# Optimization experiments

Measured on AMD Instinct MI355X. Metric: run time of the kernel, lower is better.

Reference implementation:

```python
import jax, jax.numpy as jnp
import numpy as np

B, S, HID = 1, 2048, 2048
NH, NKV, HD = 32, 8, 64
SCALE = HD ** -0.5


def _rotary_tables(seq_len, dim, base=10000.0):
    inv_freq = 1.0 / (base ** (jnp.arange(0, dim, 2, dtype=jnp.float32) / dim))
    t = jnp.arange(seq_len, dtype=jnp.float32)
    freqs = jnp.outer(t, inv_freq)                      # [S, D/2]
    emb = jnp.concatenate([freqs, freqs], axis=-1)      # [S, D]
    return jnp.cos(emb)[None], jnp.sin(emb)[None]       # [1, S, D]


def setup_inputs() -> dict:
    key = jax.random.key(0)
    ks = jax.random.split(key, 5)
    cos, sin = _rotary_tables(S, HD)
    std = HID ** -0.5
    return {
        "hidden_states": jax.random.normal(ks[0], (B, S, HID), jnp.float32),
        "cos": cos,
        "sin": sin,
        "Wq": jax.random.normal(ks[1], (HID, NH * HD), jnp.float32) * std,
        "Wk": jax.random.normal(ks[2], (HID, NKV * HD), jnp.float32) * std,
        "Wv": jax.random.normal(ks[3], (HID, NKV * HD), jnp.float32) * std,
        "Wo": jax.random.normal(ks[4], (NH * HD, HID), jnp.float32) * std,
    }


def _rotate_half(x):
    x1, x2 = jnp.split(x, 2, axis=-1)
    return jnp.concatenate([-x2, x1], axis=-1)


def reference(hidden_states, cos, sin, Wq, Wk, Wv, Wo):
    b, s, _ = hidden_states.shape
    # projections -> [B, H, S, D]
    q = (hidden_states @ Wq).reshape(b, s, NH, HD).transpose(0, 2, 1, 3)
    k = (hidden_states @ Wk).reshape(b, s, NKV, HD).transpose(0, 2, 1, 3)
    v = (hidden_states @ Wv).reshape(b, s, NKV, HD).transpose(0, 2, 1, 3)
    # rotary embedding (broadcast over heads)
    c = cos[:, None, :, :]
    sn = sin[:, None, :, :]
    q = q * c + _rotate_half(q) * sn
    k = k * c + _rotate_half(k) * sn
    # GQA: repeat kv heads
    groups = NH // NKV
    k = jnp.repeat(k, groups, axis=1)
    v = jnp.repeat(v, groups, axis=1)
    scores = jnp.einsum("bhqd,bhkd->bhqk", q, k) * SCALE
    causal = jnp.tril(jnp.ones((s, s), dtype=bool))
    scores = jnp.where(causal, scores, jnp.finfo(scores.dtype).min)
    weights = jax.nn.softmax(scores, axis=-1)
    attn = jnp.einsum("bhqk,bhkd->bhqd", weights, v)
    attn = attn.transpose(0, 2, 1, 3).reshape(b, s, NH * HD)
    out = attn @ Wo
    return out, weights
```

## Files before the change

### kernel.cpp

```cpp
#include <hip/hip_runtime.h>

typedef short short8 __attribute__((ext_vector_type(8)));
typedef float f32x4 __attribute__((ext_vector_type(4)));

#define S_LEN 2048
#define HID 2048
#define NH 32
#define NKV 8
#define HD 64
#define DQKV 3072
#define SCALE 0.125f
#define SM_OFF 8.0f

static __device__ __forceinline__ unsigned short f2bf(float f) {
    unsigned int u = __float_as_uint(f);
    u += 0x7FFF + ((u >> 16) & 1);
    return (unsigned short)(u >> 16);
}
static __device__ __forceinline__ float bf2f(unsigned short u) {
    return __uint_as_float((unsigned int)u << 16);
}

#define GLDS16(g, l)                                                                     \
    __builtin_amdgcn_global_load_lds((const __attribute__((address_space(1))) unsigned int*)(g), \
                                     (__attribute__((address_space(3))) unsigned int*)(l), 16, 0, 0)

__global__ void prep(const float* __restrict__ Wq, const float* __restrict__ Wk,
                     const float* __restrict__ Wv, const float* __restrict__ Wo,
                     const float* __restrict__ hidden,
                     unsigned short* __restrict__ Wt, unsigned short* __restrict__ Wot,
                     unsigned short* __restrict__ Hb) {
    const int z = blockIdx.z;
    const int t = threadIdx.x;
    if (z == 4) {
        int idx = (blockIdx.y * 64 + blockIdx.x) * 256 + t;
        float4 v = ((const float4*)hidden)[idx];
        ushort4 o = {f2bf(v.x), f2bf(v.y), f2bf(v.z), f2bf(v.w)};
        ((ushort4*)Hb)[idx] = o;
        return;
    }
    const float* src; unsigned short* dst; int sld;
    if (z == 0)      { src = Wq; dst = Wt; sld = HID; }
    else if (z == 1) { if (blockIdx.x >= 16) return; src = Wk; dst = Wt + (size_t)2048 * HID; sld = 512; }
    else if (z == 2) { if (blockIdx.x >= 16) return; src = Wv; dst = Wt + (size_t)2560 * HID; sld = 512; }
    else             { src = Wo; dst = Wot; sld = HID; }
    __shared__ float tile[32][33];
    const int tx = t & 31, ty = t >> 5;
    const int r0 = blockIdx.y * 32, c0 = blockIdx.x * 32;
#pragma unroll
    for (int i = 0; i < 4; ++i)
        tile[ty * 4 + i][tx] = src[(size_t)(r0 + ty * 4 + i) * sld + c0 + tx];
    __syncthreads();
#pragma unroll
    for (int i = 0; i < 4; ++i)
        dst[(size_t)(c0 + ty * 4 + i) * HID + r0 + tx] = f2bf(tile[tx][ty * 4 + i]);
}

template <int MODE>
__global__ __launch_bounds__(512) void gemm_fused(const unsigned short* __restrict__ A,
                                                  const unsigned short* __restrict__ Bt,
                                                  float* __restrict__ C,
                                                  const float* __restrict__ cosb,
                                                  const float* __restrict__ sinb,
                                                  unsigned short* __restrict__ Qb,
                                                  unsigned short* __restrict__ Kb,
                                                  unsigned short* __restrict__ Vt,
                                                  int K, int lda, int ldb, int ldc) {
    __shared__ __align__(16) unsigned short As[128 * 64];
    __shared__ __align__(16) unsigned short Bs[128 * 64];
    const int t = threadIdx.x, lane = t & 63, wv = t >> 6;
    const int m0 = blockIdx.y * 128, n0 = blockIdx.x * 128;
    const int wm = wv >> 1, wn = wv & 1;
    const int lr = lane & 15, lg = lane >> 4;
    const int srow = lane >> 3;
    const int scol = ((lane & 7) ^ srow) * 8;
    f32x4 acc[2][4] = {};
    for (int k0 = 0; k0 < K; k0 += 64) {
        __syncthreads();
#pragma unroll
        for (int p = 0; p < 2; ++p) {
            int rbase = wv * 16 + p * 8;
            GLDS16(&A[(size_t)(m0 + rbase + srow) * lda + k0 + scol], &As[rbase * 64]);
            GLDS16(&Bt[(size_t)(n0 + rbase + srow) * ldb + k0 + scol], &Bs[rbase * 64]);
        }
        __syncthreads();
#pragma unroll
        for (int kk = 0; kk < 2; ++kk) {
            short8 a[2], b[4];
#pragma unroll
            for (int i = 0; i < 2; ++i) {
                int row = wm * 32 + i * 16 + lr;
                a[i] = *(const short8*)&As[row * 64 + (((kk * 4 + lg) ^ (row & 7)) * 8)];
            }
#pragma unroll
            for (int j = 0; j < 4; ++j) {
                int row = wn * 64 + j * 16 + lr;
                b[j] = *(const short8*)&Bs[row * 64 + (((kk * 4 + lg) ^ (row & 7)) * 8)];
            }
#pragma unroll
            for (int i = 0; i < 2; ++i)
#pragma unroll
                for (int j = 0; j < 4; ++j)
                    acc[i][j] = __builtin_amdgcn_mfma_f32_16x16x32_bf16(a[i], b[j], acc[i][j], 0, 0, 0);
        }
    }

    if (MODE == 1) {
#pragma unroll
        for (int i = 0; i < 2; ++i)
#pragma unroll
            for (int j = 0; j < 4; ++j)
#pragma unroll
                for (int r = 0; r < 4; ++r)
                    C[(size_t)(m0 + wm * 32 + i * 16 + lg * 4 + r) * ldc +
                      n0 + wn * 64 + j * 16 + lr] = acc[i][j][r];
        return;
    }

    const int head = (n0 + wn * 64) >> 6;
    if (head < NH + NKV) {
        unsigned short* dst = (head < NH) ? Qb : Kb;
        const int dld = (head < NH) ? HID : 512;
        const int hc = (head < NH) ? head * HD : (head - NH) * HD;
#pragma unroll
        for (int i = 0; i < 2; ++i) {
            const int s0 = m0 + wm * 32 + i * 16 + lg * 4;
#pragma unroll
            for (int j = 0; j < 2; ++j) {
                const int c = j * 16 + lr;
#pragma unroll
                for (int r = 0; r < 4; ++r) {
                    const int s = s0 + r;
                    float x1 = acc[i][j][r], x2 = acc[i][j + 2][r];
                    float c1 = cosb[s * HD + c],      s1 = sinb[s * HD + c];
                    float c2 = cosb[s * HD + c + 32], s2 = sinb[s * HD + c + 32];
                    dst[(size_t)s * dld + hc + c]      = f2bf(x1 * c1 - x2 * s1);
                    dst[(size_t)s * dld + hc + c + 32] = f2bf(x2 * c2 + x1 * s2);
                }
            }
        }
    } else {
        const int vh = head - NH - NKV;
#pragma unroll
        for (int i = 0; i < 2; ++i) {
            const int s0 = m0 + wm * 32 + i * 16 + lg * 4;
#pragma unroll
            for (int j = 0; j < 4; ++j) {
                const int d = vh * HD + j * 16 + lr;
                ushort4 o = {f2bf(acc[i][j][0]), f2bf(acc[i][j][1]),
                             f2bf(acc[i][j][2]), f2bf(acc[i][j][3])};
                *(ushort4*)&Vt[(size_t)d * S_LEN + s0] = o;
            }
        }
    }
}

__global__ __launch_bounds__(512, 2) void attn_fused(const unsigned short* __restrict__ Qb,
                                                     const unsigned short* __restrict__ Kb,
                                                     const unsigned short* __restrict__ Vt,
                                                     float* __restrict__ w,
                                                     unsigned short* __restrict__ Ab) {
    __shared__ __align__(16) unsigned short Ks[128 * 72];
    __shared__ __align__(16) unsigned short Vs[64 * 136];
    __shared__ __align__(16) unsigned short Ps[8][32 * 40];
    const int p = blockIdx.x, h = blockIdx.y, kvh = h >> 2;
    const int t = threadIdx.x, lane = t & 63, wv = t >> 6;
    const int grp = wv & 1, wr = wv >> 1;
    const int qt = grp ? (15 - p) : p;
    const int q0 = qt * 128;
    const int lr = lane & 15, lg = lane >> 4;
    const int ktmax = 15 - p;
    unsigned short* Pw = &Ps[wv][0];

    short8 qf[2][2];
#pragma unroll
    for (int i = 0; i < 2; ++i)
#pragma unroll
        for (int kk = 0; kk < 2; ++kk)
            qf[i][kk] = *(const short8*)&Qb[(size_t)(q0 + wr * 32 + i * 16 + lr) * HID +
                                            h * HD + kk * 32 + lg * 8];

    const int krow = t >> 2, kc = (t & 3) * 16;
    const int vrow = t >> 3, vc = (t & 7) * 16;

    float l_r[2] = {0.f, 0.f};

    for (int kt = 0; kt <= ktmax; ++kt) {
        __syncthreads();
        *(short8*)&Ks[krow * 72 + kc] =
            *(const short8*)&Kb[(size_t)(kt * 128 + krow) * 512 + kvh * HD + kc];
        *(short8*)&Ks[krow * 72 + kc + 8] =
            *(const short8*)&Kb[(size_t)(kt * 128 + krow) * 512 + kvh * HD + kc + 8];
        __syncthreads();
        if (kt > qt) continue;
        f32x4 acc[8][2] = {};
#pragma unroll
        for (int kk = 0; kk < 2; ++kk) {
            short8 af[8];
#pragma unroll
            for (int j = 0; j < 8; ++j)
                af[j] = *(const short8*)&Ks[(j * 16 + lr) * 72 + kk * 32 + lg * 8];
#pragma unroll
            for (int j = 0; j < 8; ++j)
#pragma unroll
                for (int i = 0; i < 2; ++i)
                    acc[j][i] = __builtin_amdgcn_mfma_f32_16x16x32_bf16(af[j], qf[i][kk], acc[j][i], 0, 0, 0);
        }
        const bool diag = (kt == qt);
#pragma unroll
        for (int i = 0; i < 2; ++i) {
            const int qg = q0 + wr * 32 + i * 16 + lr;
            float sum = 0.f;
#pragma unroll
            for (int j = 0; j < 8; ++j)
#pragma unroll
                for (int r = 0; r < 4; ++r) {
                    int kg = kt * 128 + j * 16 + lg * 4 + r;
                    float s = acc[j][i][r] * SCALE;
                    s = (!diag || kg <= qg) ? s : -1.0e30f;
                    sum += __expf(s - SM_OFF);
                }
            sum += __shfl_xor(sum, 16);
            sum += __shfl_xor(sum, 32);
            l_r[i] += sum;
        }
    }

    const float invl[2] = {1.f / l_r[0], 1.f / l_r[1]};

    f32x4 o[2][4] = {};
    for (int kt = 0; kt <= ktmax; ++kt) {
        __syncthreads();
        *(short8*)&Ks[krow * 72 + kc] =
            *(const short8*)&Kb[(size_t)(kt * 128 + krow) * 512 + kvh * HD + kc];
        *(short8*)&Ks[krow * 72 + kc + 8] =
            *(const short8*)&Kb[(size_t)(kt * 128 + krow) * 512 + kvh * HD + kc + 8];
        *(short8*)&Vs[vrow * 136 + vc] =
            *(const short8*)&Vt[(size_t)(kvh * HD + vrow) * S_LEN + kt * 128 + vc];
        *(short8*)&Vs[vrow * 136 + vc + 8] =
            *(const short8*)&Vt[(size_t)(kvh * HD + vrow) * S_LEN + kt * 128 + vc + 8];
        __syncthreads();
        if (kt <= qt) {
            f32x4 acc[8][2] = {};
#pragma unroll
            for (int kk = 0; kk < 2; ++kk) {
                short8 af[8];
#pragma unroll
                for (int j = 0; j < 8; ++j)
                    af[j] = *(const short8*)&Ks[(j * 16 + lr) * 72 + kk * 32 + lg * 8];
#pragma unroll
                for (int j = 0; j < 8; ++j)
#pragma unroll
                    for (int i = 0; i < 2; ++i)
                        acc[j][i] = __builtin_amdgcn_mfma_f32_16x16x32_bf16(af[j], qf[i][kk], acc[j][i], 0, 0, 0);
            }
            const bool diag = (kt == qt);
#pragma unroll
            for (int ks = 0; ks < 4; ++ks) {
#pragma unroll
                for (int i = 0; i < 2; ++i) {
                    const int qg = q0 + wr * 32 + i * 16 + lr;
#pragma unroll
                    for (int jj = 0; jj < 2; ++jj) {
                        const int j = ks * 2 + jj;
                        ushort4 pk;
#pragma unroll
                        for (int r = 0; r < 4; ++r) {
                            int kg = kt * 128 + j * 16 + lg * 4 + r;
                            float s = acc[j][i][r] * SCALE;
                            s = (!diag || kg <= qg) ? s : -1.0e30f;
                            ((unsigned short*)&pk)[r] = f2bf(__expf(s - SM_OFF) * invl[i]);
                        }
                        *(ushort4*)&Pw[(i * 16 + lr) * 40 + jj * 16 + lg * 4] = pk;
                    }
                }
                short8 pa[2], vb[4];
#pragma unroll
                for (int i = 0; i < 2; ++i)
                    pa[i] = *(const short8*)&Pw[(i * 16 + lr) * 40 + lg * 8];
#pragma unroll
                for (int j2 = 0; j2 < 4; ++j2)
                    vb[j2] = *(const short8*)&Vs[(j2 * 16 + lr) * 136 + ks * 32 + lg * 8];
#pragma unroll
                for (int i = 0; i < 2; ++i)
#pragma unroll
                    for (int j2 = 0; j2 < 4; ++j2)
                        o[i][j2] = __builtin_amdgcn_mfma_f32_16x16x32_bf16(pa[i], vb[j2], o[i][j2], 0, 0, 0);
#pragma unroll
                for (int rp = 0; rp < 2; ++rp) {
                    int rq = (lane >> 2) + rp * 16;
                    int cb = (lane & 3) * 8;
                    short8 pv8 = *(const short8*)&Pw[rq * 40 + cb];
                    f32x4 f0 = {bf2f((unsigned short)pv8[0]), bf2f((unsigned short)pv8[1]),
                                bf2f((unsigned short)pv8[2]), bf2f((unsigned short)pv8[3])};
                    f32x4 f1 = {bf2f((unsigned short)pv8[4]), bf2f((unsigned short)pv8[5]),
                                bf2f((unsigned short)pv8[6]), bf2f((unsigned short)pv8[7])};
                    size_t base = ((size_t)h * S_LEN + q0 + wr * 32 + rq) * S_LEN + kt * 128 + ks * 32 + cb;
                    *(f32x4*)&w[base] = f0;
                    *(f32x4*)&w[base + 4] = f1;
                }
            }
        } else {
            f32x4 z4 = {0.f, 0.f, 0.f, 0.f};
#pragma unroll
            for (int rr = 0; rr < 16; ++rr) {
                int row = wr * 32 + rr * 2 + (lane >> 5);
                *(f32x4*)&w[((size_t)h * S_LEN + q0 + row) * S_LEN + kt * 128 + (lane & 31) * 4] = z4;
            }
        }
    }
    for (int kt = ktmax + 1; kt < 16; ++kt) {
        f32x4 z4 = {0.f, 0.f, 0.f, 0.f};
#pragma unroll
        for (int rr = 0; rr < 16; ++rr) {
            int row = wr * 32 + rr * 2 + (lane >> 5);
            *(f32x4*)&w[((size_t)h * S_LEN + q0 + row) * S_LEN + kt * 128 + (lane & 31) * 4] = z4;
        }
    }
#pragma unroll
    for (int i = 0; i < 2; ++i)
#pragma unroll
        for (int j2 = 0; j2 < 4; ++j2)
#pragma unroll
            for (int r = 0; r < 4; ++r)
                Ab[(size_t)(q0 + wr * 32 + i * 16 + lg * 4 + r) * HID +
                   h * HD + j2 * 16 + lr] = f2bf(o[i][j2][r]);
}

extern "C" void kernel_launch(void* const* d_in, const int* in_sizes, int n_in,
                              void* d_out, int out_size, void* d_ws, size_t ws_size,
                              hipStream_t stream) {
    const float* hidden = (const float*)d_in[0];
    const float* cosb   = (const float*)d_in[1];
    const float* sinb   = (const float*)d_in[2];
    const float* Wq     = (const float*)d_in[3];
    const float* Wk     = (const float*)d_in[4];
    const float* Wv     = (const float*)d_in[5];
    const float* Wo     = (const float*)d_in[6];

    float* out_mat = (float*)d_out;
    float* weights = (float*)d_out + (size_t)S_LEN * HID;

    char* wsb = (char*)d_ws;
    unsigned short* Hb  = (unsigned short*)wsb;
    unsigned short* Wt  = (unsigned short*)(wsb + (size_t)8  * 1024 * 1024);
    unsigned short* Wot = (unsigned short*)(wsb + (size_t)20 * 1024 * 1024);
    unsigned short* Qb  = (unsigned short*)(wsb + (size_t)28 * 1024 * 1024);
    unsigned short* Kb  = (unsigned short*)(wsb + (size_t)36 * 1024 * 1024);
    unsigned short* Vt  = (unsigned short*)(wsb + (size_t)38 * 1024 * 1024);
    unsigned short* Ab  = (unsigned short*)(wsb + (size_t)40 * 1024 * 1024);

    prep<<<dim3(64, 64, 5), 256, 0, stream>>>(Wq, Wk, Wv, Wo, hidden, Wt, Wot, Hb);

    gemm_fused<0><<<dim3(DQKV / 128, S_LEN / 128), 512, 0, stream>>>(
        Hb, Wt, nullptr, cosb, sinb, Qb, Kb, Vt, HID, HID, HID, 0);

    attn_fused<<<dim3(8, NH), 512, 0, stream>>>(Qb, Kb, Vt, weights, Ab);

    gemm_fused<1><<<dim3(HID / 128, S_LEN / 128), 512, 0, stream>>>(
        Ab, Wot, out_mat, nullptr, nullptr, nullptr, nullptr, nullptr, HID, HID, HID, HID);
}
```

Measured before the change: 270.4 us.

## Double-buffer K/V tiles in LDS with register prefetch in attention loops

Both attention passes now keep two LDS buffers for K (and V) and prefetch the next tile into registers while the current tile is computed. Each iteration then needs one barrier instead of two, which is meant to hide global load latency. LDS use roughly doubles and the launch bound drops its min-blocks hint of 2, so occupancy may fall and register pressure rises. The softmax exponent is also folded into an fmaf.

```diff
diff --git a/kernel.cpp b/kernel.cpp
--- a/kernel.cpp
+++ b/kernel.cpp
@@ -155,13 +155,15 @@
     }
 }
 
-__global__ __launch_bounds__(512, 2) void attn_fused(const unsigned short* __restrict__ Qb,
-                                                     const unsigned short* __restrict__ Kb,
-                                                     const unsigned short* __restrict__ Vt,
-                                                     float* __restrict__ w,
-                                                     unsigned short* __restrict__ Ab) {
-    __shared__ __align__(16) unsigned short Ks[128 * 72];
-    __shared__ __align__(16) unsigned short Vs[64 * 136];
+#define KSZ (128 * 72)
+#define VSZ (64 * 136)
+__global__ __launch_bounds__(512) void attn_fused(const unsigned short* __restrict__ Qb,
+                                                  const unsigned short* __restrict__ Kb,
+                                                  const unsigned short* __restrict__ Vt,
+                                                  float* __restrict__ w,
+                                                  unsigned short* __restrict__ Ab) {
+    __shared__ __align__(16) unsigned short Ks[2 * KSZ];
+    __shared__ __align__(16) unsigned short Vs[2 * VSZ];
     __shared__ __align__(16) unsigned short Ps[8][32 * 40];
     const int p = blockIdx.x, h = blockIdx.y, kvh = h >> 2;
     const int t = threadIdx.x, lane = t & 63, wv = t >> 6;
@@ -172,6 +174,9 @@
     const int ktmax = 15 - p;
     unsigned short* Pw = &Ps[wv][0];
 
+    const float C1 = SCALE;
+    const float NEG = -1.0e30f;
+
     short8 qf[2][2];
 #pragma unroll
     for (int i = 0; i < 2; ++i)
@@ -183,63 +188,23 @@
     const int krow = t >> 2, kc = (t & 3) * 16;
     const int vrow = t >> 3, vc = (t & 7) * 16;
 
+    short8 kA, kB, vA, vB;
+#define LOADK(kt) { const unsigned short* kp = &Kb[(size_t)((kt) * 128 + krow) * 512 + kvh * HD]; \
+                    kA = *(const short8*)&kp[kc]; kB = *(const short8*)&kp[kc + 8]; }
+#define WRITEK(b) { *(short8*)&Ks[(b) * KSZ + krow * 72 + kc] = kA;                 \
+                    *(short8*)&Ks[(b) * KSZ + krow * 72 + kc + 8] = kB; }
+#define LOADV(kt) { const unsigned short* vp = &Vt[(size_t)(kvh * HD + vrow) * S_LEN + (kt) * 128]; \
+                    vA = *(const short8*)&vp[vc]; vB = *(const short8*)&vp[vc + 8]; }
+#define WRITEV(b) { *(short8*)&Vs[(b) * VSZ + vrow * 136 + vc] = vA;                \
+                    *(short8*)&Vs[(b) * VSZ + vrow * 136 + vc + 8] = vB; }
+
     float l_r[2] = {0.f, 0.f};
 
+    LOADK(0); WRITEK(0);
+    __syncthreads();
+    LOADK(1);
     for (int kt = 0; kt <= ktmax; ++kt) {
-        __syncthreads();
-        *(short8*)&Ks[krow * 72 + kc] =
-            *(const short8*)&Kb[(size_t)(kt * 128 + krow) * 512 + kvh * HD + kc];
-        *(short8*)&Ks[krow * 72 + kc + 8] =
-            *(const short8*)&Kb[(size_t)(kt * 128 + krow) * 512 + kvh * HD + kc + 8];
-        __syncthreads();
-        if (kt > qt) continue;
-        f32x4 acc[8][2] = {};
-#pragma unroll
-        for (int kk = 0; kk < 2; ++kk) {
-            short8 af[8];
-#pragma unroll
-            for (int j = 0; j < 8; ++j)
-                af[j] = *(const short8*)&Ks[(j * 16 + lr) * 72 + kk * 32 + lg * 8];
-#pragma unroll
-            for (int j = 0; j < 8; ++j)
-#pragma unroll
-                for (int i = 0; i < 2; ++i)
-                    acc[j][i] = __builtin_amdgcn_mfma_f32_16x16x32_bf16(af[j], qf[i][kk], acc[j][i], 0, 0, 0);
-        }
-        const bool diag = (kt == qt);
-#pragma unroll
-        for (int i = 0; i < 2; ++i) {
-            const int qg = q0 + wr * 32 + i * 16 + lr;
-            float sum = 0.f;
-#pragma unroll
-            for (int j = 0; j < 8; ++j)
-#pragma unroll
-                for (int r = 0; r < 4; ++r) {
-                    int kg = kt * 128 + j * 16 + lg * 4 + r;
-                    float s = acc[j][i][r] * SCALE;
-                    s = (!diag || kg <= qg) ? s : -1.0e30f;
-                    sum += __expf(s - SM_OFF);
-                }
-            sum += __shfl_xor(sum, 16);
-            sum += __shfl_xor(sum, 32);
-            l_r[i] += sum;
-        }
-    }
-
-    const float invl[2] = {1.f / l_r[0], 1.f / l_r[1]};
-
-    f32x4 o[2][4] = {};
-    for (int kt = 0; kt <= ktmax; ++kt) {
-        __syncthreads();
-        *(short8*)&Ks[krow * 72 + kc] =
-            *(const short8*)&Kb[(size_t)(kt * 128 + krow) * 512 + kvh * HD + kc];
-        *(short8*)&Ks[krow * 72 + kc + 8] =
-            *(const short8*)&Kb[(size_t)(kt * 128 + krow) * 512 + kvh * HD + kc + 8];
-        *(short8*)&Vs[vrow * 136 + vc] =
-            *(const short8*)&Vt[(size_t)(kvh * HD + vrow) * S_LEN + kt * 128 + vc];
-        *(short8*)&Vs[vrow * 136 + vc + 8] =
-            *(const short8*)&Vt[(size_t)(kvh * HD + vrow) * S_LEN + kt * 128 + vc + 8];
-        __syncthreads();
+        const int b = kt & 1;
         if (kt <= qt) {
             f32x4 acc[8][2] = {};
 #pragma unroll
@@ -247,7 +212,53 @@
                 short8 af[8];
 #pragma unroll
                 for (int j = 0; j < 8; ++j)
-                    af[j] = *(const short8*)&Ks[(j * 16 + lr) * 72 + kk * 32 + lg * 8];
+                    af[j] = *(const short8*)&Ks[b * KSZ + (j * 16 + lr) * 72 + kk * 32 + lg * 8];
+#pragma unroll
+                for (int j = 0; j < 8; ++j)
+#pragma unroll
+                    for (int i = 0; i < 2; ++i)
+                        acc[j][i] = __builtin_amdgcn_mfma_f32_16x16x32_bf16(af[j], qf[i][kk], acc[j][i], 0, 0, 0);
+            }
+            const bool diag = (kt == qt);
+#pragma unroll
+            for (int i = 0; i < 2; ++i) {
+                const int qg = q0 + wr * 32 + i * 16 + lr;
+                float sum = 0.f;
+#pragma unroll
+                for (int j = 0; j < 8; ++j)
+#pragma unroll
+                    for (int r = 0; r < 4; ++r) {
+                        int kg = kt * 128 + j * 16 + lg * 4 + r;
+                        float s2 = fmaf(acc[j][i][r], C1, -SM_OFF);
+                        s2 = (!diag || kg <= qg) ? s2 : NEG;
+                        sum += __expf(s2);
+                    }
+                sum += __shfl_xor(sum, 16);
+                sum += __shfl_xor(sum, 32);
+                l_r[i] += sum;
+            }
+        }
+        if (kt < ktmax) WRITEK(b ^ 1);
+        __syncthreads();
+        if (kt + 2 <= ktmax) LOADK(kt + 2);
+    }
+
+    const float invl[2] = {1.f / l_r[0], 1.f / l_r[1]};
+
+    f32x4 o[2][4] = {};
+    LOADK(0); LOADV(0); WRITEK(0); WRITEV(0);
+    __syncthreads();
+    LOADK(1); LOADV(1);
+    for (int kt = 0; kt <= ktmax; ++kt) {
+        const int b = kt & 1;
+        if (kt <= qt) {
+            f32x4 acc[8][2] = {};
+#pragma unroll
+            for (int kk = 0; kk < 2; ++kk) {
+                short8 af[8];
+#pragma unroll
+                for (int j = 0; j < 8; ++j)
+                    af[j] = *(const short8*)&Ks[b * KSZ + (j * 16 + lr) * 72 + kk * 32 + lg * 8];
 #pragma unroll
                 for (int j = 0; j < 8; ++j)
 #pragma unroll
@@ -267,9 +278,9 @@
 #pragma unroll
                         for (int r = 0; r < 4; ++r) {
                             int kg = kt * 128 + j * 16 + lg * 4 + r;
-                            float s = acc[j][i][r] * SCALE;
-                            s = (!diag || kg <= qg) ? s : -1.0e30f;
-                            ((unsigned short*)&pk)[r] = f2bf(__expf(s - SM_OFF) * invl[i]);
+                            float s2 = fmaf(acc[j][i][r], C1, -SM_OFF);
+                            s2 = (!diag || kg <= qg) ? s2 : NEG;
+                            ((unsigned short*)&pk)[r] = f2bf(__expf(s2) * invl[i]);
                         }
                         *(ushort4*)&Pw[(i * 16 + lr) * 40 + jj * 16 + lg * 4] = pk;
                     }
@@ -280,7 +291,7 @@
                     pa[i] = *(const short8*)&Pw[(i * 16 + lr) * 40 + lg * 8];
 #pragma unroll
                 for (int j2 = 0; j2 < 4; ++j2)
-                    vb[j2] = *(const short8*)&Vs[(j2 * 16 + lr) * 136 + ks * 32 + lg * 8];
+                    vb[j2] = *(const short8*)&Vs[b * VSZ + (j2 * 16 + lr) * 136 + ks * 32 + lg * 8];
 #pragma unroll
                 for (int i = 0; i < 2; ++i)
 #pragma unroll
@@ -308,6 +319,9 @@
                 *(f32x4*)&w[((size_t)h * S_LEN + q0 + row) * S_LEN + kt * 128 + (lane & 31) * 4] = z4;
             }
         }
+        if (kt < ktmax) { WRITEK(b ^ 1); WRITEV(b ^ 1); }
+        __syncthreads();
+        if (kt + 2 <= ktmax) { LOADK(kt + 2); LOADV(kt + 2); }
     }
     for (int kt = ktmax + 1; kt < 16; ++kt) {
         f32x4 z4 = {0.f, 0.f, 0.f, 0.f};
```

Measured after the change: 260.8 us. -3.6%, faster.
